# Optimization experiments

Hardware: AMD Instinct MI355X
Metric: run time of the kernel (lower is better)

The kernel has to match this reference:

```python
import jax, jax.numpy as jnp
import numpy as np

DEPTH = 3
B, D, O = 8192, 1024, 1024
HR = 32            # router hidden
HE = 2 * D         # expert hidden
N_NODES = 2 ** DEPTH - 1
N_LEAVES = 2 ** DEPTH


def setup_inputs() -> dict:
    key = jax.random.key(0)
    ks = jax.random.split(key, 9)
    x = jax.random.normal(ks[0], (B, D), dtype=jnp.float32)
    # decision-node router params (stacked over nodes)
    rW1 = jax.random.normal(ks[1], (N_NODES, D, HR), dtype=jnp.float32) * 0.05
    rb1 = jnp.zeros((N_NODES, HR), dtype=jnp.float32)
    rW2 = jax.random.normal(ks[2], (N_NODES, HR, 2), dtype=jnp.float32) * 0.05
    rb2 = jnp.zeros((N_NODES, 2), dtype=jnp.float32)
    # leaf-expert params (stacked over experts)
    eW1 = jax.random.normal(ks[3], (N_LEAVES, D, HE), dtype=jnp.float32) * 0.02
    eb1 = jnp.zeros((N_LEAVES, HE), dtype=jnp.float32)
    eW2 = jax.random.normal(ks[4], (N_LEAVES, HE, O), dtype=jnp.float32) * 0.02
    eb2 = jnp.zeros((N_LEAVES, O), dtype=jnp.float32)
    return {"x": x, "rW1": rW1, "rb1": rb1, "rW2": rW2, "rb2": rb2,
            "eW1": eW1, "eb1": eb1, "eW2": eW2, "eb2": eb2, "top_k": 4}


def _gelu(v):
    return jax.nn.gelu(v, approximate=False)  # torch nn.GELU default = exact erf


def _leaf_probs(x, rW1, rb1, rW2, rb2):
    # all decision nodes batched: [N, B, 2]
    h = _gelu(jnp.einsum('bd,ndh->nbh', x, rW1) + rb1[:, None, :])
    logits = jnp.einsum('nbh,nhc->nbc', h, rW2) + rb2[:, None, :]
    dec = jax.nn.softmax(logits, axis=-1)
    # BFS product of path probabilities, level by level (fixed small loop)
    probs = jnp.ones((x.shape[0], 1), dtype=x.dtype)
    start = 0
    for level in range(DEPTH):
        w = 2 ** level
        dl = dec[start:start + w].transpose(1, 0, 2)       # [B, w, 2]
        probs = (probs[:, :, None] * dl).reshape(x.shape[0], 2 * w)
        start += w
    return probs  # [B, N_LEAVES]


def reference(x, rW1, rb1, rW2, rb2, eW1, eb1, eW2, eb2, top_k):
    leaf_probs = _leaf_probs(x, rW1, rb1, rW2, rb2)
    if top_k is not None and top_k < N_LEAVES:
        vals, idx = jax.lax.top_k(leaf_probs, top_k)       # [B, k]
        sparse = jnp.zeros_like(leaf_probs)
        sparse = sparse.at[jnp.arange(leaf_probs.shape[0])[:, None], idx].set(vals)
        leaf_probs = sparse / (sparse.sum(axis=1, keepdims=True) + 1e-8)
    # all leaf experts, batched (dense weighted sum; skip heuristic is an approximation)
    h = _gelu(jnp.einsum('bd,edh->ebh', x, eW1) + eb1[:, None, :])   # [E, B, HE]
    out = jnp.einsum('ebh,eho->ebo', h, eW2) + eb2[:, None, :]        # [E, B, O]
    y = jnp.einsum('ebo,be->bo', out, leaf_probs)
    return (y, leaf_probs)
```

## Files before the change

kernel.cpp:

```cpp
#include <hip/hip_runtime.h>
#include <hip/hip_bf16.h>
#include <cstdint>

#define B_   8192
#define D_   1024
#define O_   1024
#define HE_  2048
#define NN_  7
#define NL_  8
#define HR_  32
#define RC_  224
#define K3_  3072
#define MTMAX_ 264

typedef __attribute__((ext_vector_type(2))) float f32x2;
typedef __attribute__((ext_vector_type(4))) float f32x4;
typedef __attribute__((ext_vector_type(8))) short bf16x8;
typedef __attribute__((ext_vector_type(4))) unsigned short u16x4;
typedef unsigned short u16;
typedef unsigned int u32;

__device__ __forceinline__ u16 f2bf(float f) {
  __hip_bfloat16 h = __float2bfloat16(f);
  return *reinterpret_cast<u16*>(&h);
}
__device__ __forceinline__ float bf2f(u16 u) {
  u32 v = ((u32)u) << 16;
  return *reinterpret_cast<float*>(&v);
}
__device__ __forceinline__ float gelu_exact(float v) {
  return 0.5f * v * (1.0f + erff(v * 0.7071067811865475f));
}
__device__ __forceinline__ void gload16(const void* g, void* l) {
  __builtin_amdgcn_global_load_lds(
      (const __attribute__((address_space(1))) void*)(uintptr_t)g,
      (__attribute__((address_space(3))) void*)(uintptr_t)l,
      16, 0, 0);
}

__global__ __launch_bounds__(256) void build_xbs_kernel(
    const float* __restrict__ in, u16* __restrict__ out) {
  size_t i = ((size_t)blockIdx.x * 256 + threadIdx.x) * 4;
  size_t row = i >> 10;
  int col = (int)(i & 1023);
  f32x4 f = *reinterpret_cast<const f32x4*>(in + i);
  u16x4 hi, lo;
#pragma unroll
  for (int j = 0; j < 4; j++) {
    hi[j] = f2bf(f[j]);
    lo[j] = f2bf(f[j] - bf2f(hi[j]));
  }
  u16* base = out + row * 2048 + col;
  *reinterpret_cast<u16x4*>(base)        = hi;
  *reinterpret_cast<u16x4*>(base + 1024) = lo;
}

__global__ __launch_bounds__(256) void build_wr3_kernel(
    const float* __restrict__ rW1, u16* __restrict__ Wr3) {
  size_t i = ((size_t)blockIdx.x * 256 + threadIdx.x) * 4;
  int c = (int)(i / K3_), k = (int)(i % K3_);
  int j = k >> 10, kk = k & 1023;
  u16x4 o;
  if (c < RC_) {
    int node = c >> 5, h = c & 31;
    const float* src = rW1 + ((size_t)node * 1024 + kk) * HR_ + h;
#pragma unroll
    for (int t = 0; t < 4; t++) {
      float f = src[t * HR_];
      u16 hi = f2bf(f);
      o[t] = (j == 1) ? f2bf(f - bf2f(hi)) : hi;
    }
  } else {
    o[0] = 0; o[1] = 0; o[2] = 0; o[3] = 0;
  }
  *reinterpret_cast<u16x4*>(Wr3 + i) = o;
}

__global__ __launch_bounds__(256) void transpose_cvt_kernel(
    const float* __restrict__ in, u16* __restrict__ out,
    int R, int C, int ldo, long in_estride, long out_estride) {
  __shared__ __attribute__((aligned(16))) float tile[64][65];
  const float* in_e = in + (long)blockIdx.z * in_estride;
  u16* out_e = out + (long)blockIdx.z * out_estride;
  int t = threadIdx.x;
  int r0 = blockIdx.y * 64, c0 = blockIdx.x * 64;
  int cc = t & 63, rbase = t >> 6;
#pragma unroll
  for (int i = 0; i < 16; i++) {
    int rr = rbase + i * 4;
    tile[rr][cc] = in_e[(long)(r0 + rr) * C + c0 + cc];
  }
  __syncthreads();
  int r2 = (t & 31) * 2, cj = t >> 5;
#pragma unroll
  for (int i = 0; i < 8; i++) {
    int c = cj * 8 + i;
    u32 u = (u32)f2bf(tile[r2][c]) | ((u32)f2bf(tile[r2 + 1][c]) << 16);
    *reinterpret_cast<u32*>(out_e + (long)(c0 + c) * ldo + r0 + r2) = u;
  }
}

__global__ __launch_bounds__(256, 2) void router_gemm_kernel(
    const u16* __restrict__ Xbs, const u16* __restrict__ Bm,
    float* __restrict__ H1p) {
  __shared__ __attribute__((aligned(16))) u16 lA[128 * 32];
  __shared__ __attribute__((aligned(16))) u16 lB[128 * 32];
  int tid = threadIdx.x;
  int gid = blockIdx.x;
  int cpx = gridDim.x >> 3;
  gid = (gid & 7) * cpx + (gid >> 3);
  int s = gid >> 7;
  int rem = gid & 127;
  int band = rem >> 4, inb = rem & 15;
  long m0 = (long)(band * 8 + (inb & 7)) * 128;
  long n0 = (long)(inb >> 3) * 128;
  int wid = tid >> 6, lane = tid & 63;
  int wm = wid >> 1, wn = wid & 1;
  f32x4 acc[4][4];
#pragma unroll
  for (int m = 0; m < 4; m++)
#pragma unroll
    for (int n = 0; n < 4; n++) acc[m][n] = (f32x4){0.f, 0.f, 0.f, 0.f};
  int lr = lane & 15, lk = (lane >> 4) * 8;
  int srow = tid >> 2, soff = (tid & 3) * 8;
  const u16* Bb = Bm + n0 * K3_;
  int kbeg = s * 768, kend = kbeg + 768;
  for (int k0 = kbeg; k0 < kend; k0 += 32) {
    int ca = (k0 < 1024) ? k0 : k0 - 1024;
    gload16(Xbs + (m0 + srow) * 2048 + ca + soff, &lA[tid * 8]);
    gload16(Xbs + (m0 + 64 + srow) * 2048 + ca + soff, &lA[(256 + tid) * 8]);
    gload16(Bb + (long)srow * K3_ + k0 + soff, &lB[tid * 8]);
    gload16(Bb + (long)(64 + srow) * K3_ + k0 + soff, &lB[(256 + tid) * 8]);
    __syncthreads();
    bf16x8 af[4], bfr[4];
#pragma unroll
    for (int m = 0; m < 4; m++)
      af[m] = *reinterpret_cast<const bf16x8*>(&lA[(wm * 64 + m * 16 + lr) * 32 + lk]);
#pragma unroll
    for (int n = 0; n < 4; n++)
      bfr[n] = *reinterpret_cast<const bf16x8*>(&lB[(wn * 64 + n * 16 + lr) * 32 + lk]);
#pragma unroll
    for (int m = 0; m < 4; m++)
#pragma unroll
      for (int n = 0; n < 4; n++)
        acc[m][n] = __builtin_amdgcn_mfma_f32_16x16x32_bf16(af[m], bfr[n], acc[m][n], 0, 0, 0);
    __syncthreads();
  }
  int lq = lane >> 4;
#pragma unroll
  for (int m = 0; m < 4; m++)
#pragma unroll
    for (int n = 0; n < 4; n++)
#pragma unroll
      for (int j = 0; j < 4; j++) {
        long row = m0 + wm * 64 + m * 16 + lq * 4 + j;
        long col = n0 + wn * 64 + n * 16 + lr;
        if (col < RC_)
          H1p[((long)s * B_ + row) * RC_ + col] = acc[m][n][j];
      }
}

__global__ __launch_bounds__(256) void router_logits_kernel(
    const float* __restrict__ H1p, const float* __restrict__ rb1,
    const float* __restrict__ rW2, const float* __restrict__ rb2,
    const int* __restrict__ topk_ptr, float* __restrict__ P) {
  int b = blockIdx.x * 256 + threadIdx.x;
  float dec[NN_][2];
#pragma unroll
  for (int n = 0; n < NN_; n++) {
    float l0 = rb2[n * 2], l1 = rb2[n * 2 + 1];
#pragma unroll
    for (int r4 = 0; r4 < HR_; r4 += 4) {
      int c = n * HR_ + r4;
      f32x4 hs = *reinterpret_cast<const f32x4*>(&H1p[((long)0 * B_ + b) * RC_ + c]);
#pragma unroll
      for (int s = 1; s < 4; s++)
        hs += *reinterpret_cast<const f32x4*>(&H1p[((long)s * B_ + b) * RC_ + c]);
      f32x4 bv = *reinterpret_cast<const f32x4*>(rb1 + c);
#pragma unroll
      for (int j = 0; j < 4; j++) {
        float hv = gelu_exact(hs[j] + bv[j]);
        l0 += hv * rW2[(c + j) * 2];
        l1 += hv * rW2[(c + j) * 2 + 1];
      }
    }
    float mx = fmaxf(l0, l1);
    float e0 = expf(l0 - mx), e1 = expf(l1 - mx);
    float sm = e0 + e1;
    dec[n][0] = e0 / sm; dec[n][1] = e1 / sm;
  }
  float v[NL_];
#pragma unroll
  for (int L = 0; L < NL_; L++)
    v[L] = dec[0][L >> 2] * dec[1 + (L >> 2)][(L >> 1) & 1] * dec[3 + (L >> 1)][L & 1];
  int tk = *topk_ptr;
  float p[NL_];
  if (tk < NL_) {
    float s = 0.f;
    bool keep[NL_];
#pragma unroll
    for (int e = 0; e < NL_; e++) {
      int rank = 0;
#pragma unroll
      for (int j = 0; j < NL_; j++)
        rank += ((v[j] > v[e]) || (v[j] == v[e] && j < e)) ? 1 : 0;
      keep[e] = rank < tk;
      if (keep[e]) s += v[e];
    }
    float inv = 1.f / (s + 1e-8f);
#pragma unroll
    for (int e = 0; e < NL_; e++) p[e] = keep[e] ? v[e] * inv : 0.f;
  } else {
#pragma unroll
    for (int e = 0; e < NL_; e++) p[e] = v[e];
  }
#pragma unroll
  for (int e = 0; e < NL_; e++) P[(long)b * NL_ + e] = p[e];
}

__global__ __launch_bounds__(256) void yinit_kernel(
    const float* __restrict__ P, const float* __restrict__ eb2,
    float* __restrict__ y) {
  size_t i = ((size_t)blockIdx.x * 256 + threadIdx.x) * 4;
  size_t row = i >> 10;
  int col = (int)(i & 1023);
  f32x4 s = (f32x4){0.f, 0.f, 0.f, 0.f};
#pragma unroll
  for (int e = 0; e < NL_; e++) {
    float pe = P[row * NL_ + e];
    f32x4 w = *reinterpret_cast<const f32x4*>(eb2 + (size_t)e * O_ + col);
    s += w * pe;
  }
  *reinterpret_cast<f32x4*>(y + i) = s;
}

__global__ __launch_bounds__(256) void compact_kernel(
    const float* __restrict__ P, int* __restrict__ idx,
    int* __restrict__ counts) {
  int e = blockIdx.x, t = threadIdx.x;
  __shared__ int sc[256];
  __shared__ int sbase;
  if (t == 0) sbase = 0;
  __syncthreads();
  for (int c0 = 0; c0 < B_; c0 += 256) {
    int r = c0 + t;
    int f = (P[(long)r * NL_ + e] > 0.f) ? 1 : 0;
    sc[t] = f;
    __syncthreads();
#pragma unroll
    for (int d = 1; d < 256; d <<= 1) {
      int v = (t >= d) ? sc[t - d] : 0;
      __syncthreads();
      sc[t] += v;
      __syncthreads();
    }
    int pos = sbase + sc[t] - 1;
    int tot = sc[255];
    if (f) idx[(long)e * B_ + pos] = r;
    __syncthreads();
    if (t == 0) sbase += tot;
    __syncthreads();
  }
  if (t == 0) counts[e] = sbase;
}

__global__ void tiles_kernel(const int* __restrict__ counts,
                             int* __restrict__ toff) {
  int s = 0;
#pragma unroll
  for (int e = 0; e < NL_; e++) { toff[e] = s; s += (counts[e] + 127) >> 7; }
  toff[NL_] = s;
}

__global__ __launch_bounds__(256, 2) void gemme1_kernel(
    const u16* __restrict__ Xbs, const u16* __restrict__ W1t,
    const float* __restrict__ eb1, const float* __restrict__ P,
    u16* __restrict__ Hall, const int* __restrict__ idx,
    const int* __restrict__ counts, const int* __restrict__ toff) {
  __shared__ __attribute__((aligned(16))) u16 lA[128 * 64];
  __shared__ __attribute__((aligned(16))) u16 lB[128 * 64];
  int tid = threadIdx.x;
  int gid = blockIdx.x;
  int cpx = gridDim.x >> 3;
  gid = (gid & 7) * cpx + (gid >> 3);
  int mt = gid >> 4, nt = gid & 15;
  if (mt >= toff[NL_]) return;
  int e = 0;
#pragma unroll
  for (int f = 1; f < NL_; f++) e += (mt >= toff[f]) ? 1 : 0;
  int cnt = counts[e];
  long m0 = (long)(mt - toff[e]) * 128;
  long n0 = (long)nt * 128;
  const int* idxe = idx + (long)e * B_;
  int wid = tid >> 6, lane = tid & 63;
  int wm = wid >> 1, wn = wid & 1;
  f32x4 acc[4][4];
#pragma unroll
  for (int m = 0; m < 4; m++)
#pragma unroll
    for (int n = 0; n < 4; n++) acc[m][n] = (f32x4){0.f, 0.f, 0.f, 0.f};
  int lr = lane & 15, lkg = lane >> 4;
  const u16* gA[4]; const u16* gB[4]; int lds_o[4];
  const u16* Bb = W1t + ((size_t)e * HE_ + n0) * D_;
#pragma unroll
  for (int i = 0; i < 4; i++) {
    int sidx = tid + i * 256;
    int r = sidx >> 3, j = sidx & 7;
    int so = ((j ^ (r & 7)) << 3);
    int gi = (m0 + r < cnt) ? idxe[m0 + r] : 0;
    gA[i] = Xbs + (long)gi * 2048 + so;
    gB[i] = Bb + (long)r * D_ + so;
    lds_o[i] = sidx * 8;
  }
  int foA[4][2], foB[4][2];
#pragma unroll
  for (int m = 0; m < 4; m++) {
    int r = wm * 64 + m * 16 + lr;
#pragma unroll
    for (int kk = 0; kk < 2; kk++)
      foA[m][kk] = r * 128 + ((((kk * 4 + lkg) ^ (r & 7))) << 4);
  }
#pragma unroll
  for (int n = 0; n < 4; n++) {
    int r = wn * 64 + n * 16 + lr;
#pragma unroll
    for (int kk = 0; kk < 2; kk++)
      foB[n][kk] = r * 128 + ((((kk * 4 + lkg) ^ (r & 7))) << 4);
  }
  const char* pa = (const char*)lA;
  const char* pb = (const char*)lB;
  for (int k0 = 0; k0 < D_; k0 += 64) {
#pragma unroll
    for (int i = 0; i < 4; i++) gload16(gA[i] + k0, &lA[lds_o[i]]);
#pragma unroll
    for (int i = 0; i < 4; i++) gload16(gB[i] + k0, &lB[lds_o[i]]);
    __syncthreads();
    bf16x8 af[4][2], bfr[4][2];
#pragma unroll
    for (int m = 0; m < 4; m++) {
      af[m][0] = *reinterpret_cast<const bf16x8*>(pa + foA[m][0]);
      af[m][1] = *reinterpret_cast<const bf16x8*>(pa + foA[m][1]);
    }
#pragma unroll
    for (int n = 0; n < 4; n++) {
      bfr[n][0] = *reinterpret_cast<const bf16x8*>(pb + foB[n][0]);
      bfr[n][1] = *reinterpret_cast<const bf16x8*>(pb + foB[n][1]);
    }
#pragma unroll
    for (int m = 0; m < 4; m++)
#pragma unroll
      for (int n = 0; n < 4; n++) {
        acc[m][n] = __builtin_amdgcn_mfma_f32_16x16x32_bf16(af[m][0], bfr[n][0], acc[m][n], 0, 0, 0);
        acc[m][n] = __builtin_amdgcn_mfma_f32_16x16x32_bf16(af[m][1], bfr[n][1], acc[m][n], 0, 0, 0);
      }
    __syncthreads();
  }
  int lq = lane >> 4;
  long hbase = (long)toff[e] * 128;
#pragma unroll
  for (int m = 0; m < 4; m++) {
#pragma unroll
    for (int j = 0; j < 4; j++) {
      long lrow = m0 + wm * 64 + m * 16 + lq * 4 + j;
      if (lrow >= cnt) continue;
      int orow = idxe[lrow];
      float pw = P[(long)orow * NL_ + e];
#pragma unroll
      for (int n = 0; n < 4; n++) {
        long col = n0 + wn * 64 + n * 16 + lr;
        float g = gelu_exact(acc[m][n][j] + eb1[(size_t)e * HE_ + col]);
        Hall[(hbase + lrow) * HE_ + col] = f2bf(g * pw);
      }
    }
  }
}

__global__ __launch_bounds__(256, 2) void gemme2_kernel(
    const u16* __restrict__ Hall, const u16* __restrict__ W2t,
    float* __restrict__ y, const int* __restrict__ idx,
    const int* __restrict__ counts, const int* __restrict__ toff) {
  __shared__ __attribute__((aligned(16))) u16 lA[128 * 64];
  __shared__ __attribute__((aligned(16))) u16 lB[128 * 64];
  int tid = threadIdx.x;
  int gid = blockIdx.x;
  int cpx = gridDim.x >> 3;
  gid = (gid & 7) * cpx + (gid >> 3);
  int mt = gid >> 3, nt = gid & 7;
  if (mt >= toff[NL_]) return;
  int e = 0;
#pragma unroll
  for (int f = 1; f < NL_; f++) e += (mt >= toff[f]) ? 1 : 0;
  int cnt = counts[e];
  long m0 = (long)(mt - toff[e]) * 128;
  long n0 = (long)nt * 128;
  const int* idxe = idx + (long)e * B_;
  int wid = tid >> 6, lane = tid & 63;
  int wm = wid >> 1, wn = wid & 1;
  f32x4 acc[4][4];
#pragma unroll
  for (int m = 0; m < 4; m++)
#pragma unroll
    for (int n = 0; n < 4; n++) acc[m][n] = (f32x4){0.f, 0.f, 0.f, 0.f};
  int lr = lane & 15, lkg = lane >> 4;
  const u16* Ab = Hall + ((long)toff[e] * 128 + m0) * HE_;
  const u16* Bb = W2t + ((size_t)e * O_ + n0) * HE_;
  const u16* gA[4]; const u16* gB[4]; int lds_o[4];
#pragma unroll
  for (int i = 0; i < 4; i++) {
    int sidx = tid + i * 256;
    int r = sidx >> 3, j = sidx & 7;
    int so = ((j ^ (r & 7)) << 3);
    gA[i] = Ab + (long)r * HE_ + so;
    gB[i] = Bb + (long)r * HE_ + so;
    lds_o[i] = sidx * 8;
  }
  int foA[4][2], foB[4][2];
#pragma unroll
  for (int m = 0; m < 4; m++) {
    int r = wm * 64 + m * 16 + lr;
#pragma unroll
    for (int kk = 0; kk < 2; kk++)
      foA[m][kk] = r * 128 + ((((kk * 4 + lkg) ^ (r & 7))) << 4);
  }
#pragma unroll
  for (int n = 0; n < 4; n++) {
    int r = wn * 64 + n * 16 + lr;
#pragma unroll
    for (int kk = 0; kk < 2; kk++)
      foB[n][kk] = r * 128 + ((((kk * 4 + lkg) ^ (r & 7))) << 4);
  }
  const char* pa = (const char*)lA;
  const char* pb = (const char*)lB;
  for (int k0 = 0; k0 < HE_; k0 += 64) {
#pragma unroll
    for (int i = 0; i < 4; i++) gload16(gA[i] + k0, &lA[lds_o[i]]);
#pragma unroll
    for (int i = 0; i < 4; i++) gload16(gB[i] + k0, &lB[lds_o[i]]);
    __syncthreads();
    bf16x8 af[4][2], bfr[4][2];
#pragma unroll
    for (int m = 0; m < 4; m++) {
      af[m][0] = *reinterpret_cast<const bf16x8*>(pa + foA[m][0]);
      af[m][1] = *reinterpret_cast<const bf16x8*>(pa + foA[m][1]);
    }
#pragma unroll
    for (int n = 0; n < 4; n++) {
      bfr[n][0] = *reinterpret_cast<const bf16x8*>(pb + foB[n][0]);
      bfr[n][1] = *reinterpret_cast<const bf16x8*>(pb + foB[n][1]);
    }
#pragma unroll
    for (int m = 0; m < 4; m++)
#pragma unroll
      for (int n = 0; n < 4; n++) {
        acc[m][n] = __builtin_amdgcn_mfma_f32_16x16x32_bf16(af[m][0], bfr[n][0], acc[m][n], 0, 0, 0);
        acc[m][n] = __builtin_amdgcn_mfma_f32_16x16x32_bf16(af[m][1], bfr[n][1], acc[m][n], 0, 0, 0);
      }
    __syncthreads();
  }
  int lq = lane >> 4;
#pragma unroll
  for (int m = 0; m < 4; m++) {
#pragma unroll
    for (int j = 0; j < 4; j++) {
      long lrow = m0 + wm * 64 + m * 16 + lq * 4 + j;
      if (lrow >= cnt) continue;
      long orow = idxe[lrow];
#pragma unroll
      for (int n = 0; n < 4; n++) {
        long col = n0 + wn * 64 + n * 16 + lr;
        unsafeAtomicAdd(&y[orow * O_ + col], acc[m][n][j]);
      }
    }
  }
}

extern "C" void kernel_launch(void* const* d_in, const int* in_sizes, int n_in,
                              void* d_out, int out_size, void* d_ws, size_t ws_size,
                              hipStream_t stream) {
  (void)in_sizes; (void)n_in; (void)out_size; (void)ws_size;
  const float* x   = (const float*)d_in[0];
  const float* rW1 = (const float*)d_in[1];
  const float* rb1 = (const float*)d_in[2];
  const float* rW2 = (const float*)d_in[3];
  const float* rb2 = (const float*)d_in[4];
  const float* eW1 = (const float*)d_in[5];
  const float* eb1 = (const float*)d_in[6];
  const float* eW2 = (const float*)d_in[7];
  const float* eb2 = (const float*)d_in[8];
  const int*  topk = (const int*)d_in[9];
  float* y = (float*)d_out;
  float* P = y + (size_t)B_ * O_;

  char* ws = (char*)d_ws;
  u16*  Xbs = (u16*)ws;
  u16*  W1t = (u16*)(ws + 33554432);
  u16*  W2t = (u16*)(ws + 67108864);
  int*  idx    = (int*)(ws + 100663296);
  int*  counts = (int*)(ws + 100925440);
  int*  toff   = (int*)(ws + 100925504);
  char* hreg   = ws + 100925952;
  u16*  Hall = (u16*)hreg;
  u16*  Wr3  = (u16*)hreg;
  float* H1p = (float*)(hreg + 2097152);

  build_xbs_kernel<<<(B_ * D_) / 1024, 256, 0, stream>>>(x, Xbs);
  build_wr3_kernel<<<(256 * K3_) / 1024, 256, 0, stream>>>(rW1, Wr3);
  transpose_cvt_kernel<<<dim3(HE_ / 64, D_ / 64, NL_), 256, 0, stream>>>(
      eW1, W1t, D_, HE_, D_, (long)D_ * HE_, (long)HE_ * D_);
  transpose_cvt_kernel<<<dim3(O_ / 64, HE_ / 64, NL_), 256, 0, stream>>>(
      eW2, W2t, HE_, O_, HE_, (long)HE_ * O_, (long)O_ * HE_);
  router_gemm_kernel<<<512, 256, 0, stream>>>(Xbs, Wr3, H1p);
  router_logits_kernel<<<B_ / 256, 256, 0, stream>>>(H1p, rb1, rW2, rb2, topk, P);
  yinit_kernel<<<(B_ * O_) / 1024, 256, 0, stream>>>(P, eb2, y);
  compact_kernel<<<NL_, 256, 0, stream>>>(P, idx, counts);
  tiles_kernel<<<1, 1, 0, stream>>>(counts, toff);

  gemme1_kernel<<<MTMAX_ * 16, 256, 0, stream>>>(
      Xbs, W1t, eb1, P, Hall, idx, counts, toff);
  gemme2_kernel<<<MTMAX_ * 8, 256, 0, stream>>>(
      Hall, W2t, y, idx, counts, toff);
}
```

Before: 669.6 us.

## Double-buffer LDS tiles in expert GEMMs to overlap loads with MFMA

```diff
diff --git a/kernel.cpp b/kernel.cpp
--- a/kernel.cpp
+++ b/kernel.cpp
@@ -37,6 +37,10 @@
       (__attribute__((address_space(3))) void*)(uintptr_t)l,
       16, 0, 0);
 }
+#define WAITVM0   asm volatile("s_waitcnt vmcnt(0)" ::: "memory")
+#define WAITLGKM0 do { \
+  asm volatile("s_waitcnt lgkmcnt(0)" ::: "memory"); \
+  __builtin_amdgcn_sched_barrier(0); } while (0)
 
 __global__ __launch_bounds__(256) void build_xbs_kernel(
     const float* __restrict__ in, u16* __restrict__ out) {
@@ -277,8 +281,8 @@
     const float* __restrict__ eb1, const float* __restrict__ P,
     u16* __restrict__ Hall, const int* __restrict__ idx,
     const int* __restrict__ counts, const int* __restrict__ toff) {
-  __shared__ __attribute__((aligned(16))) u16 lA[128 * 64];
-  __shared__ __attribute__((aligned(16))) u16 lB[128 * 64];
+  __shared__ __attribute__((aligned(16))) u16 lA[2][128 * 64];
+  __shared__ __attribute__((aligned(16))) u16 lB[2][128 * 64];
   int tid = threadIdx.x;
   int gid = blockIdx.x;
   int cpx = gridDim.x >> 3;
@@ -327,14 +331,20 @@
     for (int kk = 0; kk < 2; kk++)
       foB[n][kk] = r * 128 + ((((kk * 4 + lkg) ^ (r & 7))) << 4);
   }
-  const char* pa = (const char*)lA;
-  const char* pb = (const char*)lB;
-  for (int k0 = 0; k0 < D_; k0 += 64) {
-#pragma unroll
-    for (int i = 0; i < 4; i++) gload16(gA[i] + k0, &lA[lds_o[i]]);
-#pragma unroll
-    for (int i = 0; i < 4; i++) gload16(gB[i] + k0, &lB[lds_o[i]]);
-    __syncthreads();
+#define STAGE1(buf, k0) do { _Pragma("unroll") \
+  for (int i_ = 0; i_ < 4; i_++) gload16(gA[i_] + (k0), &lA[buf][lds_o[i_]]); \
+  _Pragma("unroll") \
+  for (int i_ = 0; i_ < 4; i_++) gload16(gB[i_] + (k0), &lB[buf][lds_o[i_]]); \
+  } while (0)
+  STAGE1(0, 0);
+  WAITVM0;
+  __builtin_amdgcn_s_barrier();
+  int cur = 0;
+  constexpr int NT = D_ / 64;
+  for (int t = 0; t < NT; ++t) {
+    if (t + 1 < NT) STAGE1(cur ^ 1, (t + 1) * 64);
+    const char* pa = (const char*)lA[cur];
+    const char* pb = (const char*)lB[cur];
     bf16x8 af[4][2], bfr[4][2];
 #pragma unroll
     for (int m = 0; m < 4; m++) {
@@ -346,6 +356,8 @@
       bfr[n][0] = *reinterpret_cast<const bf16x8*>(pb + foB[n][0]);
       bfr[n][1] = *reinterpret_cast<const bf16x8*>(pb + foB[n][1]);
     }
+    WAITLGKM0;
+    __builtin_amdgcn_s_setprio(1);
 #pragma unroll
     for (int m = 0; m < 4; m++)
 #pragma unroll
@@ -353,8 +365,12 @@
         acc[m][n] = __builtin_amdgcn_mfma_f32_16x16x32_bf16(af[m][0], bfr[n][0], acc[m][n], 0, 0, 0);
         acc[m][n] = __builtin_amdgcn_mfma_f32_16x16x32_bf16(af[m][1], bfr[n][1], acc[m][n], 0, 0, 0);
       }
-    __syncthreads();
-  }
+    __builtin_amdgcn_s_setprio(0);
+    WAITVM0;
+    __builtin_amdgcn_s_barrier();
+    cur ^= 1;
+  }
+#undef STAGE1
   int lq = lane >> 4;
   long hbase = (long)toff[e] * 128;
 #pragma unroll
@@ -379,8 +395,8 @@
     const u16* __restrict__ Hall, const u16* __restrict__ W2t,
     float* __restrict__ y, const int* __restrict__ idx,
     const int* __restrict__ counts, const int* __restrict__ toff) {
-  __shared__ __attribute__((aligned(16))) u16 lA[128 * 64];
-  __shared__ __attribute__((aligned(16))) u16 lB[128 * 64];
+  __shared__ __attribute__((aligned(16))) u16 lA[2][128 * 64];
+  __shared__ __attribute__((aligned(16))) u16 lB[2][128 * 64];
   int tid = threadIdx.x;
   int gid = blockIdx.x;
   int cpx = gridDim.x >> 3;
@@ -429,14 +445,20 @@
     for (int kk = 0; kk < 2; kk++)
       foB[n][kk] = r * 128 + ((((kk * 4 + lkg) ^ (r & 7))) << 4);
   }
-  const char* pa = (const char*)lA;
-  const char* pb = (const char*)lB;
-  for (int k0 = 0; k0 < HE_; k0 += 64) {
-#pragma unroll
-    for (int i = 0; i < 4; i++) gload16(gA[i] + k0, &lA[lds_o[i]]);
-#pragma unroll
-    for (int i = 0; i < 4; i++) gload16(gB[i] + k0, &lB[lds_o[i]]);
-    __syncthreads();
+#define STAGE2(buf, k0) do { _Pragma("unroll") \
+  for (int i_ = 0; i_ < 4; i_++) gload16(gA[i_] + (k0), &lA[buf][lds_o[i_]]); \
+  _Pragma("unroll") \
+  for (int i_ = 0; i_ < 4; i_++) gload16(gB[i_] + (k0), &lB[buf][lds_o[i_]]); \
+  } while (0)
+  STAGE2(0, 0);
+  WAITVM0;
+  __builtin_amdgcn_s_barrier();
+  int cur = 0;
+  constexpr int NT = HE_ / 64;
+  for (int t = 0; t < NT; ++t) {
+    if (t + 1 < NT) STAGE2(cur ^ 1, (t + 1) * 64);
+    const char* pa = (const char*)lA[cur];
+    const char* pb = (const char*)lB[cur];
     bf16x8 af[4][2], bfr[4][2];
 #pragma unroll
     for (int m = 0; m < 4; m++) {
@@ -448,6 +470,8 @@
       bfr[n][0] = *reinterpret_cast<const bf16x8*>(pb + foB[n][0]);
       bfr[n][1] = *reinterpret_cast<const bf16x8*>(pb + foB[n][1]);
     }
+    WAITLGKM0;
+    __builtin_amdgcn_s_setprio(1);
 #pragma unroll
     for (int m = 0; m < 4; m++)
 #pragma unroll
@@ -455,8 +479,12 @@
         acc[m][n] = __builtin_amdgcn_mfma_f32_16x16x32_bf16(af[m][0], bfr[n][0], acc[m][n], 0, 0, 0);
         acc[m][n] = __builtin_amdgcn_mfma_f32_16x16x32_bf16(af[m][1], bfr[n][1], acc[m][n], 0, 0, 0);
       }
-    __syncthreads();
-  }
+    __builtin_amdgcn_s_setprio(0);
+    WAITVM0;
+    __builtin_amdgcn_s_barrier();
+    cur ^= 1;
+  }
+#undef STAGE2
   int lq = lane >> 4;
 #pragma unroll
   for (int m = 0; m < 4; m++) {
```

After: 720.5 us. +7.6%, slower.
